# Performance work log

Hardware: AMD Instinct MI355X
Metric: run time of the kernel (lower is better)

Reference implementation:

```python
import jax, jax.numpy as jnp
import numpy as np

# Correlation2D hyperparameters (FlowNet-style cost volume, corr_multiply=1)
PAD = 3          # pad_size
K = 3            # kernel_size (odd)
MD = 1           # max_displacement
S1 = 1           # stride1 (output stride)
S2 = 1           # stride2 (displacement stride)
KR = (K - 1) // 2            # kernel radius
GR = MD // S2                # neighborhood grid radius
D = 2 * GR + 1               # displacements per axis -> D*D output channels


def setup_inputs() -> dict:
    key = jax.random.key(0)
    k1, k2 = jax.random.split(key)
    B, C, H, W = 4, 96, 256, 256
    input1 = jax.random.normal(k1, (B, C, H, W), dtype=jnp.float32)
    input2 = jax.random.normal(k2, (B, C, H, W), dtype=jnp.float32)
    return {"input1": input1, "input2": input2}


def _correlation(x1, x2):
    B, C, H, W = x1.shape
    p1 = jnp.pad(x1, ((0, 0), (0, 0), (PAD, PAD), (PAD, PAD)))
    p2 = jnp.pad(x2, ((0, 0), (0, 0), (PAD, PAD), (PAD, PAD)))
    Hp, Wp = H + 2 * PAD, W + 2 * PAD
    # patch centers y1 = y*S1 + MD + KR; output size per FlowNet corr_cuda
    Ho = (Hp - 2 * KR - 2 * MD - 1) // S1 + 1
    Wo = (Wp - 2 * KR - 2 * MD - 1) // S1 + 1
    # extra pad so shifted slices of p2 are always in-bounds (zeros never read)
    p2e = jnp.pad(p2, ((0, 0), (0, 0), (MD, MD), (MD, MD)))
    box = jnp.ones((1, 1, K, K), x1.dtype)
    norm = jnp.asarray(K * K * C, x1.dtype)
    outs = []
    for tj in range(-GR, GR + 1):       # channel order: (tj+GR)*D + (ti+GR)
        for ti in range(-GR, GR + 1):
            dy, dx = tj * S2, ti * S2
            shifted = p2e[:, :, MD + dy:MD + dy + Hp, MD + dx:MD + dx + Wp]
            # channel-summed pointwise product: (B,1,Hp,Wp)
            q = jnp.sum(p1 * shifted, axis=1, keepdims=True)
            # K x K box window sum (VALID): index o = top-left = y1-KR
            s = jax.lax.conv_general_dilated(q, box, (1, 1), 'VALID')
            # window top-left for output y is y*S1 + MD
            s = s[:, 0, MD:MD + (Ho - 1) * S1 + 1:S1, MD:MD + (Wo - 1) * S1 + 1:S1]
            outs.append(s)
    return jnp.stack(outs, axis=1) / norm   # (B, D*D, Ho, Wo)


def reference(input1, input2):
    return _correlation(input1, input2)
```

## Files before the change

kernel.cpp:

```cpp
#include <hip/hip_runtime.h>

#define HC 256
#define WC 256
#define CC 96
#define BB 4
#define OH 258
#define OW 258
#define PLANE 65536
#define NPAIR 128
#define NW 8
#define CGW 12
#define K2_JOBS (BB * 9 * OH)
#define K2_BLOCKS ((K2_JOBS + 3) / 4)
#define WS_NEEDED ((size_t)BB * 9 * PLANE * 4)

__device__ __forceinline__ float4 ld4(const float* p){ return *reinterpret_cast<const float4*>(p); }
__device__ __forceinline__ void st4(float* p, float4 v){ *reinterpret_cast<float4*>(p) = v; }

__device__ __forceinline__ void tap6(float4& A, float4& B, float4& C, const float4 a,
                                     float w0, float w1, float w2, float w3, float w4, float w5)
{
    A.x = fmaf(a.x, w0, A.x); A.y = fmaf(a.y, w1, A.y); A.z = fmaf(a.z, w2, A.z); A.w = fmaf(a.w, w3, A.w);
    B.x = fmaf(a.x, w1, B.x); B.y = fmaf(a.y, w2, B.y); B.z = fmaf(a.z, w3, B.z); B.w = fmaf(a.w, w4, B.w);
    C.x = fmaf(a.x, w2, C.x); C.y = fmaf(a.y, w3, C.y); C.z = fmaf(a.z, w4, C.z); C.w = fmaf(a.w, w5, C.w);
}

__global__ __launch_bounds__(512) void corr_r_kernel(
    const float* __restrict__ x1, const float* __restrict__ x2, float* __restrict__ rws)
{
    const int tid = threadIdx.x;
    const int g   = tid >> 6;
    const int t   = tid & 63;
    const int bid  = blockIdx.x;
    const int pair = (bid & 7) * (NPAIR / 8) + (bid >> 3);
    const int b    = blockIdx.y;
    const int h0 = 2 * pair, h1 = h0 + 1;
    const int wq = 4 * t;

    const bool vm1 = (h0 > 0);
    const bool vp2 = (h1 < HC - 1);
    const int rm1 = vm1 ? h0 - 1 : 0;
    const int rp2 = vp2 ? h1 + 1 : HC - 1;

    const float* p1b = x1 + (size_t)(b * CC + g * CGW) * PLANE;
    const float* p2b = x2 + (size_t)(b * CC + g * CGW) * PLANE;

    const int o1a = h0 * WC + wq, o1b = h1 * WC + wq;
    const int o20 = rm1 * WC + wq, o21 = h0 * WC + wq, o22 = h1 * WC + wq, o23 = rp2 * WC + wq;

    const float4 fz = make_float4(0.f, 0.f, 0.f, 0.f);
    float4 acc0[9], acc1[9];
#pragma unroll
    for (int d = 0; d < 9; ++d) { acc0[d] = fz; acc1[d] = fz; }

    float4 A0[2], A1[2], Q0[2], Q1[2], Q2[2], Q3[2];

#define ISSUE(s, cc)                                                           \
    do {                                                                       \
        const float* P1 = p1b + (size_t)(cc) * PLANE;                          \
        const float* P2 = p2b + (size_t)(cc) * PLANE;                          \
        A0[s] = ld4(P1 + o1a);                                                 \
        A1[s] = ld4(P1 + o1b);                                                 \
        Q0[s] = vm1 ? ld4(P2 + o20) : fz;                                      \
        Q1[s] = ld4(P2 + o21);                                                 \
        Q2[s] = ld4(P2 + o22);                                                 \
        Q3[s] = vp2 ? ld4(P2 + o23) : fz;                                      \
    } while (0)

#define COMPUTE_STEP(s)                                                                          \
    do {                                                                                         \
        float pw0 = __shfl_up(Q0[s].w, 1), nx0 = __shfl_down(Q0[s].x, 1);                        \
        float pw1 = __shfl_up(Q1[s].w, 1), nx1 = __shfl_down(Q1[s].x, 1);                        \
        float pw2 = __shfl_up(Q2[s].w, 1), nx2 = __shfl_down(Q2[s].x, 1);                        \
        float pw3 = __shfl_up(Q3[s].w, 1), nx3 = __shfl_down(Q3[s].x, 1);                        \
        if (t == 0)  { pw0 = 0; pw1 = 0; pw2 = 0; pw3 = 0; }                                     \
        if (t == 63) { nx0 = 0; nx1 = 0; nx2 = 0; nx3 = 0; }                                     \
        tap6(acc0[0], acc0[1], acc0[2], A0[s], pw0, Q0[s].x, Q0[s].y, Q0[s].z, Q0[s].w, nx0);    \
        tap6(acc0[3], acc0[4], acc0[5], A0[s], pw1, Q1[s].x, Q1[s].y, Q1[s].z, Q1[s].w, nx1);    \
        tap6(acc1[0], acc1[1], acc1[2], A1[s], pw1, Q1[s].x, Q1[s].y, Q1[s].z, Q1[s].w, nx1);    \
        tap6(acc0[6], acc0[7], acc0[8], A0[s], pw2, Q2[s].x, Q2[s].y, Q2[s].z, Q2[s].w, nx2);    \
        tap6(acc1[3], acc1[4], acc1[5], A1[s], pw2, Q2[s].x, Q2[s].y, Q2[s].z, Q2[s].w, nx2);    \
        tap6(acc1[6], acc1[7], acc1[8], A1[s], pw3, Q3[s].x, Q3[s].y, Q3[s].z, Q3[s].w, nx3);    \
    } while (0)

    ISSUE(0, 0);
    ISSUE(1, 1);
#pragma unroll 2
    for (int c = 0; c < CGW; ++c) {
        const int s = c & 1;
        COMPUTE_STEP(s);
        if (c + 2 < CGW) ISSUE(s, c + 2);
    }
#undef ISSUE
#undef COMPUTE_STEP

    __shared__ __align__(16) float buf[2][9][2][WC];

#define WBUF(i)                                                              \
    do {                                                                     \
        _Pragma("unroll")                                                    \
        for (int d = 0; d < 9; ++d) {                                        \
            st4(&buf[i][d][0][wq], acc0[d]);                                 \
            st4(&buf[i][d][1][wq], acc1[d]);                                 \
        }                                                                    \
    } while (0)
#define ABUF(i)                                                              \
    do {                                                                     \
        _Pragma("unroll")                                                    \
        for (int d = 0; d < 9; ++d) {                                        \
            float4 v0 = ld4(&buf[i][d][0][wq]);                              \
            float4 v1 = ld4(&buf[i][d][1][wq]);                              \
            acc0[d].x += v0.x; acc0[d].y += v0.y;                            \
            acc0[d].z += v0.z; acc0[d].w += v0.w;                            \
            acc1[d].x += v1.x; acc1[d].y += v1.y;                            \
            acc1[d].z += v1.z; acc1[d].w += v1.w;                            \
        }                                                                    \
    } while (0)

    if (g == 1) WBUF(0);
    if (g == 5) WBUF(1);
    __syncthreads();
    if (g == 0) ABUF(0);
    if (g == 4) ABUF(1);
    __syncthreads();
    if (g == 3) WBUF(0);
    if (g == 7) WBUF(1);
    __syncthreads();
    if (g == 2) ABUF(0);
    if (g == 6) ABUF(1);
    __syncthreads();
    if (g == 2) WBUF(0);
    if (g == 6) WBUF(1);
    __syncthreads();
    if (g == 0) ABUF(0);
    if (g == 4) ABUF(1);
    __syncthreads();
    if (g == 4) WBUF(0);
    __syncthreads();

    if (g == 0) {
        ABUF(0);
#pragma unroll
        for (int d = 0; d < 9; ++d) {
            float* base = rws + (((size_t)(b * 9 + d) * HC) + h0) * WC;
            st4(base + wq, acc0[d]);
            st4(base + WC + wq, acc1[d]);
        }
    }
#undef WBUF
#undef ABUF
}

__global__ __launch_bounds__(256) void corr_box_kernel(
    const float* __restrict__ rws, float* __restrict__ out)
{
    const int tid = threadIdx.x;
    const int wid = tid >> 6, t = tid & 63;
    const int job = blockIdx.x * 4 + wid;
    if (job >= K2_JOBS) return;
    const int y  = job % OH;
    const int bd = job / OH;
    const float* rp = rws + (size_t)bd * PLANE;

    float4 s4 = make_float4(0.f, 0.f, 0.f, 0.f);
    float s256 = 0.f, s257 = 0.f;
#pragma unroll
    for (int k = 0; k < 3; ++k) {
        const int rr = y - 2 + k;
        if ((unsigned)rr < (unsigned)HC) {
            float4 q = ld4(rp + rr * WC + 4 * t);
            float pz = __shfl_up(q.z, 1);
            float pw = __shfl_up(q.w, 1);
            if (t == 0) { pz = 0.f; pw = 0.f; }
            s4.x += pz + pw + q.x;
            s4.y += pw + q.x + q.y;
            s4.z += q.x + q.y + q.z;
            s4.w += q.y + q.z + q.w;
            s256 += q.z + q.w;
            s257 += q.w;
        }
    }
    float* orow = out + ((size_t)bd * OH + y) * OW;
    const float sc = 1.0f / 864.0f;
    orow[4 * t]     = s4.x * sc;
    orow[4 * t + 1] = s4.y * sc;
    orow[4 * t + 2] = s4.z * sc;
    orow[4 * t + 3] = s4.w * sc;
    if (t == 63) { orow[256] = s256 * sc; orow[257] = s257 * sc; }
}

#define FBTOX 30
#define FBTOY 14
__global__ __launch_bounds__(256) void corr2d_fb(
    const float* __restrict__ x1, const float* __restrict__ x2, float* __restrict__ out)
{
    const int tx = threadIdx.x, ty = threadIdx.y;
    const int bx = blockIdx.x, by = blockIdx.y, b = blockIdx.z;
    const int x0 = bx * FBTOX, y0 = by * FBTOY;
    const int w = x0 - 2 + tx;
    const int h0 = y0 - 2 + ty, h1 = h0 + 8;
    const size_t plane = (size_t)HC * WC;
    const float* p1 = x1 + (size_t)b * CC * plane;
    const float* p2 = x2 + (size_t)b * CC * plane;
    float acc[2][9];
#pragma unroll
    for (int i = 0; i < 2; ++i)
#pragma unroll
        for (int d = 0; d < 9; ++d) acc[i][d] = 0.f;
    const bool interior = (x0 >= 3) && (x0 + 30 <= WC - 1) && (y0 >= 3) && (y0 + 14 <= HC - 1);
    if (interior) {
        const float* q1 = p1 + (size_t)(h0 * WC + w);
        const float* q2 = p2 + (size_t)(h0 * WC + w);
        for (int c = 0; c < CC; ++c) {
            const float a0 = q1[0];
            const float a1 = q1[8 * WC];
#pragma unroll
            for (int tj = -1; tj <= 1; ++tj)
#pragma unroll
                for (int ti = -1; ti <= 1; ++ti) {
                    const int d = (tj + 1) * 3 + (ti + 1);
                    acc[0][d] = fmaf(a0, q2[tj * WC + ti], acc[0][d]);
                    acc[1][d] = fmaf(a1, q2[(tj + 8) * WC + ti], acc[1][d]);
                }
            q1 += plane; q2 += plane;
        }
    } else {
        int rows[6]; bool rv[6];
        const int hh[6] = {h0 - 1, h0, h0 + 1, h1 - 1, h1, h1 + 1};
#pragma unroll
        for (int j = 0; j < 6; ++j) {
            rv[j] = ((unsigned)hh[j] < (unsigned)HC);
            int hcl = hh[j] < 0 ? 0 : (hh[j] > HC - 1 ? HC - 1 : hh[j]);
            rows[j] = hcl * WC;
        }
        int cols[3]; bool cv[3];
#pragma unroll
        for (int i = 0; i < 3; ++i) {
            int ww = w - 1 + i;
            cv[i] = ((unsigned)ww < (unsigned)WC);
            cols[i] = ww < 0 ? 0 : (ww > WC - 1 ? WC - 1 : ww);
        }
        const bool v0 = ((unsigned)h0 < (unsigned)HC) && ((unsigned)w < (unsigned)WC);
        const bool v1 = ((unsigned)h1 < (unsigned)HC) && ((unsigned)w < (unsigned)WC);
        const int wcl = w < 0 ? 0 : (w > WC - 1 ? WC - 1 : w);
        const int off1_0 = (h0 < 0 ? 0 : (h0 > HC - 1 ? HC - 1 : h0)) * WC + wcl;
        const int off1_1 = (h1 < 0 ? 0 : (h1 > HC - 1 ? HC - 1 : h1)) * WC + wcl;
        const float* q1 = p1;
        const float* q2 = p2;
        for (int c = 0; c < CC; ++c) {
            const float a0 = v0 ? q1[off1_0] : 0.f;
            const float a1 = v1 ? q1[off1_1] : 0.f;
#pragma unroll
            for (int jr = 0; jr < 3; ++jr)
#pragma unroll
                for (int i = 0; i < 3; ++i) {
                    const int d = jr * 3 + i;
                    const float u0 = (rv[jr] && cv[i])     ? q2[rows[jr] + cols[i]]     : 0.f;
                    const float u1 = (rv[jr + 3] && cv[i]) ? q2[rows[jr + 3] + cols[i]] : 0.f;
                    acc[0][d] = fmaf(a0, u0, acc[0][d]);
                    acc[1][d] = fmaf(a1, u1, acc[1][d]);
                }
            q1 += plane; q2 += plane;
        }
    }
    __shared__ float rl[9][16][32];
#pragma unroll
    for (int d = 0; d < 9; ++d) {
        rl[d][ty][tx]     = acc[0][d];
        rl[d][ty + 8][tx] = acc[1][d];
    }
    __syncthreads();
    const int tid = ty * 32 + tx;
    for (int j = tid; j < FBTOX * FBTOY; j += 256) {
        const int oy = j / FBTOX, ox = j - oy * FBTOX;
        const int y = y0 + oy, x = x0 + ox;
        if (y < OH && x < OW) {
#pragma unroll
            for (int d = 0; d < 9; ++d) {
                float s = 0.f;
#pragma unroll
                for (int a = 0; a < 3; ++a)
#pragma unroll
                    for (int b2 = 0; b2 < 3; ++b2)
                        s += rl[d][oy + a][ox + b2];
                out[(((size_t)b * 9 + d) * OH + y) * OW + x] = s * (1.0f / 864.0f);
            }
        }
    }
}

extern "C" void kernel_launch(void* const* d_in, const int* in_sizes, int n_in,
                              void* d_out, int out_size, void* d_ws, size_t ws_size,
                              hipStream_t stream) {
    const float* x1 = (const float*)d_in[0];
    const float* x2 = (const float*)d_in[1];
    float* out = (float*)d_out;
    if (ws_size >= WS_NEEDED) {
        float* rws = (float*)d_ws;
        hipLaunchKernelGGL(corr_r_kernel, dim3(NPAIR, BB), dim3(512), 0, stream, x1, x2, rws);
        hipLaunchKernelGGL(corr_box_kernel, dim3(K2_BLOCKS), dim3(256), 0, stream, rws, out);
    } else {
        hipLaunchKernelGGL(corr2d_fb,
                           dim3((OW + FBTOX - 1) / FBTOX, (OH + FBTOY - 1) / FBTOY, BB),
                           dim3(32, 8), 0, stream, x1, x2, out);
    }
}
```

Before: 47.78 us.

## Process four output rows per block with fewer warps and wider channel groups

```diff
diff --git a/kernel.cpp b/kernel.cpp
--- a/kernel.cpp
+++ b/kernel.cpp
@@ -7,9 +7,8 @@
 #define OH 258
 #define OW 258
 #define PLANE 65536
-#define NPAIR 128
-#define NW 8
-#define CGW 12
+#define NQUAD 64
+#define CGW 24
 #define K2_JOBS (BB * 9 * OH)
 #define K2_BLOCKS ((K2_JOBS + 3) / 4)
 #define WS_NEEDED ((size_t)BB * 9 * PLANE * 4)
@@ -25,62 +24,75 @@
     C.x = fmaf(a.x, w2, C.x); C.y = fmaf(a.y, w3, C.y); C.z = fmaf(a.z, w4, C.z); C.w = fmaf(a.w, w5, C.w);
 }
 
-__global__ __launch_bounds__(512) void corr_r_kernel(
+__global__ __launch_bounds__(256, 2) void corr_r_kernel(
     const float* __restrict__ x1, const float* __restrict__ x2, float* __restrict__ rws)
 {
     const int tid = threadIdx.x;
     const int g   = tid >> 6;
     const int t   = tid & 63;
     const int bid  = blockIdx.x;
-    const int pair = (bid & 7) * (NPAIR / 8) + (bid >> 3);
+    const int quad = (bid & 7) * (NQUAD / 8) + (bid >> 3);
     const int b    = blockIdx.y;
-    const int h0 = 2 * pair, h1 = h0 + 1;
+    const int h0 = 4 * quad;
     const int wq = 4 * t;
 
-    const bool vm1 = (h0 > 0);
-    const bool vp2 = (h1 < HC - 1);
-    const int rm1 = vm1 ? h0 - 1 : 0;
-    const int rp2 = vp2 ? h1 + 1 : HC - 1;
+    const bool vm = (h0 > 0);
+    const bool vp = (h0 + 4 < HC);
+    const int rm = vm ? h0 - 1 : 0;
+    const int rp = vp ? h0 + 4 : HC - 1;
 
     const float* p1b = x1 + (size_t)(b * CC + g * CGW) * PLANE;
     const float* p2b = x2 + (size_t)(b * CC + g * CGW) * PLANE;
 
-    const int o1a = h0 * WC + wq, o1b = h1 * WC + wq;
-    const int o20 = rm1 * WC + wq, o21 = h0 * WC + wq, o22 = h1 * WC + wq, o23 = rp2 * WC + wq;
+    const int o1_0 = h0 * WC + wq,       o1_1 = (h0 + 1) * WC + wq;
+    const int o1_2 = (h0 + 2) * WC + wq, o1_3 = (h0 + 3) * WC + wq;
+    const int o2_0 = rm * WC + wq,       o2_5 = rp * WC + wq;
 
     const float4 fz = make_float4(0.f, 0.f, 0.f, 0.f);
-    float4 acc0[9], acc1[9];
-#pragma unroll
-    for (int d = 0; d < 9; ++d) { acc0[d] = fz; acc1[d] = fz; }
-
-    float4 A0[2], A1[2], Q0[2], Q1[2], Q2[2], Q3[2];
+    float4 acc[4][9];
+#pragma unroll
+    for (int i = 0; i < 4; ++i)
+#pragma unroll
+        for (int d = 0; d < 9; ++d) acc[i][d] = fz;
+
+    float4 A[2][4], Q[2][6];
 
 #define ISSUE(s, cc)                                                           \
     do {                                                                       \
         const float* P1 = p1b + (size_t)(cc) * PLANE;                          \
         const float* P2 = p2b + (size_t)(cc) * PLANE;                          \
-        A0[s] = ld4(P1 + o1a);                                                 \
-        A1[s] = ld4(P1 + o1b);                                                 \
-        Q0[s] = vm1 ? ld4(P2 + o20) : fz;                                      \
-        Q1[s] = ld4(P2 + o21);                                                 \
-        Q2[s] = ld4(P2 + o22);                                                 \
-        Q3[s] = vp2 ? ld4(P2 + o23) : fz;                                      \
+        A[s][0] = ld4(P1 + o1_0);                                              \
+        A[s][1] = ld4(P1 + o1_1);                                              \
+        A[s][2] = ld4(P1 + o1_2);                                              \
+        A[s][3] = ld4(P1 + o1_3);                                              \
+        Q[s][0] = vm ? ld4(P2 + o2_0) : fz;                                    \
+        Q[s][1] = ld4(P2 + o1_0);                                              \
+        Q[s][2] = ld4(P2 + o1_1);                                              \
+        Q[s][3] = ld4(P2 + o1_2);                                              \
+        Q[s][4] = ld4(P2 + o1_3);                                              \
+        Q[s][5] = vp ? ld4(P2 + o2_5) : fz;                                    \
     } while (0)
 
-#define COMPUTE_STEP(s)                                                                          \
-    do {                                                                                         \
-        float pw0 = __shfl_up(Q0[s].w, 1), nx0 = __shfl_down(Q0[s].x, 1);                        \
-        float pw1 = __shfl_up(Q1[s].w, 1), nx1 = __shfl_down(Q1[s].x, 1);                        \
-        float pw2 = __shfl_up(Q2[s].w, 1), nx2 = __shfl_down(Q2[s].x, 1);                        \
-        float pw3 = __shfl_up(Q3[s].w, 1), nx3 = __shfl_down(Q3[s].x, 1);                        \
-        if (t == 0)  { pw0 = 0; pw1 = 0; pw2 = 0; pw3 = 0; }                                     \
-        if (t == 63) { nx0 = 0; nx1 = 0; nx2 = 0; nx3 = 0; }                                     \
-        tap6(acc0[0], acc0[1], acc0[2], A0[s], pw0, Q0[s].x, Q0[s].y, Q0[s].z, Q0[s].w, nx0);    \
-        tap6(acc0[3], acc0[4], acc0[5], A0[s], pw1, Q1[s].x, Q1[s].y, Q1[s].z, Q1[s].w, nx1);    \
-        tap6(acc1[0], acc1[1], acc1[2], A1[s], pw1, Q1[s].x, Q1[s].y, Q1[s].z, Q1[s].w, nx1);    \
-        tap6(acc0[6], acc0[7], acc0[8], A0[s], pw2, Q2[s].x, Q2[s].y, Q2[s].z, Q2[s].w, nx2);    \
-        tap6(acc1[3], acc1[4], acc1[5], A1[s], pw2, Q2[s].x, Q2[s].y, Q2[s].z, Q2[s].w, nx2);    \
-        tap6(acc1[6], acc1[7], acc1[8], A1[s], pw3, Q3[s].x, Q3[s].y, Q3[s].z, Q3[s].w, nx3);    \
+#define COMPUTE_STEP(s)                                                        \
+    do {                                                                       \
+        float pw[6], nx[6];                                                    \
+        _Pragma("unroll")                                                      \
+        for (int j = 0; j < 6; ++j) {                                          \
+            pw[j] = __shfl_up(Q[s][j].w, 1);                                   \
+            nx[j] = __shfl_down(Q[s][j].x, 1);                                 \
+            if (t == 0)  pw[j] = 0.f;                                          \
+            if (t == 63) nx[j] = 0.f;                                          \
+        }                                                                      \
+        _Pragma("unroll")                                                      \
+        for (int i = 0; i < 4; ++i) {                                          \
+            _Pragma("unroll")                                                  \
+            for (int k = 0; k < 3; ++k) {                                      \
+                const int j = i + k;                      \
+                tap6(acc[i][3 * k], acc[i][3 * k + 1], acc[i][3 * k + 2],      \
+                     A[s][i], pw[j], Q[s][j].x, Q[s][j].y, Q[s][j].z,          \
+                     Q[s][j].w, nx[j]);                                        \
+            }                                                                  \
+        }                                                                      \
     } while (0)
 
     ISSUE(0, 0);
@@ -96,56 +108,48 @@
 
     __shared__ __align__(16) float buf[2][9][2][WC];
 
-#define WBUF(i)                                                              \
+#define WBUF(i, ra, rb)                                                      \
     do {                                                                     \
         _Pragma("unroll")                                                    \
         for (int d = 0; d < 9; ++d) {                                        \
-            st4(&buf[i][d][0][wq], acc0[d]);                                 \
-            st4(&buf[i][d][1][wq], acc1[d]);                                 \
+            st4(&buf[i][d][0][wq], acc[ra][d]);                              \
+            st4(&buf[i][d][1][wq], acc[rb][d]);                              \
         }                                                                    \
     } while (0)
-#define ABUF(i)                                                              \
+#define ABUF(i, ra, rb)                                                      \
     do {                                                                     \
         _Pragma("unroll")                                                    \
         for (int d = 0; d < 9; ++d) {                                        \
             float4 v0 = ld4(&buf[i][d][0][wq]);                              \
             float4 v1 = ld4(&buf[i][d][1][wq]);                              \
-            acc0[d].x += v0.x; acc0[d].y += v0.y;                            \
-            acc0[d].z += v0.z; acc0[d].w += v0.w;                            \
-            acc1[d].x += v1.x; acc1[d].y += v1.y;                            \
-            acc1[d].z += v1.z; acc1[d].w += v1.w;                            \
+            acc[ra][d].x += v0.x; acc[ra][d].y += v0.y;                      \
+            acc[ra][d].z += v0.z; acc[ra][d].w += v0.w;                      \
+            acc[rb][d].x += v1.x; acc[rb][d].y += v1.y;                      \
+            acc[rb][d].z += v1.z; acc[rb][d].w += v1.w;                      \
         }                                                                    \
     } while (0)
 
-    if (g == 1) WBUF(0);
-    if (g == 5) WBUF(1);
-    __syncthreads();
-    if (g == 0) ABUF(0);
-    if (g == 4) ABUF(1);
-    __syncthreads();
-    if (g == 3) WBUF(0);
-    if (g == 7) WBUF(1);
-    __syncthreads();
-    if (g == 2) ABUF(0);
-    if (g == 6) ABUF(1);
-    __syncthreads();
-    if (g == 2) WBUF(0);
-    if (g == 6) WBUF(1);
-    __syncthreads();
-    if (g == 0) ABUF(0);
-    if (g == 4) ABUF(1);
-    __syncthreads();
-    if (g == 4) WBUF(0);
-    __syncthreads();
-
-    if (g == 0) {
-        ABUF(0);
-#pragma unroll
-        for (int d = 0; d < 9; ++d) {
-            float* base = rws + (((size_t)(b * 9 + d) * HC) + h0) * WC;
-            st4(base + wq, acc0[d]);
-            st4(base + WC + wq, acc1[d]);
-        }
+#pragma unroll
+    for (int half = 0; half < 2; ++half) {
+        const int ra = 2 * half, rb = 2 * half + 1;
+        if (g == 1) WBUF(0, ra, rb);
+        if (g == 3) WBUF(1, ra, rb);
+        __syncthreads();
+        if (g == 0) ABUF(0, ra, rb);
+        if (g == 2) ABUF(1, ra, rb);
+        __syncthreads();
+        if (g == 2) WBUF(0, ra, rb);
+        __syncthreads();
+        if (g == 0) {
+            ABUF(0, ra, rb);
+#pragma unroll
+            for (int d = 0; d < 9; ++d) {
+                float* base = rws + (((size_t)(b * 9 + d) * HC) + h0 + ra) * WC;
+                st4(base + wq, acc[ra][d]);
+                st4(base + WC + wq, acc[rb][d]);
+            }
+        }
+        __syncthreads();
     }
 #undef WBUF
 #undef ABUF
@@ -297,7 +301,7 @@
     float* out = (float*)d_out;
     if (ws_size >= WS_NEEDED) {
         float* rws = (float*)d_ws;
-        hipLaunchKernelGGL(corr_r_kernel, dim3(NPAIR, BB), dim3(512), 0, stream, x1, x2, rws);
+        hipLaunchKernelGGL(corr_r_kernel, dim3(NQUAD, BB), dim3(256), 0, stream, x1, x2, rws);
         hipLaunchKernelGGL(corr_box_kernel, dim3(K2_BLOCKS), dim3(256), 0, stream, rws, out);
     } else {
         hipLaunchKernelGGL(corr2d_fb,
```

Result: slower. 173.0 us (+262.0%).
